# Performance work log

Hardware: AMD Instinct MI355X
Metric: run time of the kernel (lower is better)

## Reference

```python
import jax, jax.numpy as jnp
import numpy as np

N_NODES = 100000
N_EDGES = 1600000
IN_DIM = 128
HID = 32
HEADS = 4
NUM_CLASS = 2


def setup_inputs() -> dict:
    key = jax.random.key(0)
    ks = jax.random.split(key, 10)
    x = jax.random.normal(ks[0], (N_NODES, IN_DIM), dtype=jnp.float32)
    edge_index = jax.random.randint(ks[1], (2, N_EDGES), 0, N_NODES, dtype=jnp.int64)
    s_in = 1.0 / np.sqrt(IN_DIM)
    s_h = 1.0 / np.sqrt(HEADS * HID)
    return {
        "x": x,
        "edge_index": edge_index,
        "W1": jax.random.normal(ks[2], (HEADS * HID, IN_DIM), dtype=jnp.float32) * s_in,
        "att_src1": jax.random.normal(ks[3], (HEADS, HID), dtype=jnp.float32) * s_in,
        "att_dst1": jax.random.normal(ks[4], (HEADS, HID), dtype=jnp.float32) * s_in,
        "b1": jnp.zeros((HEADS * HID,), dtype=jnp.float32),
        "W2": jax.random.normal(ks[5], (NUM_CLASS, HEADS * HID), dtype=jnp.float32) * s_h,
        "att_src2": jax.random.normal(ks[6], (1, NUM_CLASS), dtype=jnp.float32) * s_h,
        "att_dst2": jax.random.normal(ks[7], (1, NUM_CLASS), dtype=jnp.float32) * s_h,
        "b2": jnp.zeros((NUM_CLASS,), dtype=jnp.float32),
    }


def gat_conv(x, src, dst, W, att_src, att_dst, b, n):
    """PyG-style GATConv (self-loops already included in src/dst)."""
    H, C = att_src.shape
    h = (x @ W.T).reshape(n, H, C)                      # [N,H,C]
    a_s = jnp.einsum('nhc,hc->nh', h, att_src)           # [N,H]
    a_d = jnp.einsum('nhc,hc->nh', h, att_dst)           # [N,H]
    e = jax.nn.leaky_relu(a_s[src] + a_d[dst], 0.2)      # [E,H]
    m = jax.ops.segment_max(e, dst, num_segments=n)      # per-dst max
    m = jnp.where(jnp.isfinite(m), m, 0.0)
    ex = jnp.exp(e - m[dst])
    denom = jax.ops.segment_sum(ex, dst, num_segments=n)
    alpha = ex / (denom[dst] + 1e-16)                    # segment softmax
    out = jax.ops.segment_sum(h[src] * alpha[..., None], dst, num_segments=n)
    return out.reshape(n, H * C) + b


def reference(x, edge_index, W1, att_src1, att_dst1, b1, W2, att_src2, att_dst2, b2):
    n = x.shape[0]
    loops = jnp.arange(n, dtype=edge_index.dtype)
    ei = jnp.concatenate([edge_index, jnp.stack([loops, loops])], axis=1)
    src, dst = ei[0], ei[1]
    h = gat_conv(x, src, dst, W1, att_src1, att_dst1, b1, n)
    h = jax.nn.leaky_relu(h, 0.01)  # F.leaky_relu default slope
    # F.dropout with p=0.0 -> identity
    out = gat_conv(h, src, dst, W2, att_src2, att_dst2, b2, n)
    return jax.nn.log_softmax(out, axis=1)
```

## Files before the change

### kernel.cpp

```cpp
#include <hip/hip_runtime.h>

#define NN 100000
#define NE 1600000
#define NTOT (NN + NE)
#define NB 782
#define ACHUNK 4096
#define NCH 391
#define BCAP 3072

typedef __attribute__((ext_vector_type(8))) short bf16x8;
typedef __attribute__((ext_vector_type(4))) float f32x4;

static __device__ __forceinline__ float blo(unsigned int u) {
  union { unsigned int i; float f; } v; v.i = u << 16; return v.f;
}
static __device__ __forceinline__ float bhi(unsigned int u) {
  union { unsigned int i; float f; } v; v.i = u & 0xffff0000u; return v.f;
}
static __device__ __forceinline__ unsigned short f2bf(float f) {
  union { float f; unsigned int i; } v; v.f = f;
  unsigned int i = v.i;
  i += 0x7fffu + ((i >> 16) & 1u);
  return (unsigned short)(i >> 16);
}

__global__ __launch_bounds__(512) void kb_hist(const int* __restrict__ ei,
                                               int* __restrict__ cntMat) {
  __shared__ int h[NB];
  int tid = threadIdx.x, blk = blockIdx.x;
  int e0 = blk * ACHUNK;
  int n = min(ACHUNK, NE - e0);
  for (int i = tid; i < NB; i += 512) h[i] = 0;
  __syncthreads();
  for (int i = tid; i < n; i += 512) atomicAdd(&h[ei[NE + e0 + i] >> 7], 1);
  __syncthreads();
  for (int i = tid; i < NB; i += 512) cntMat[blk * NB + i] = h[i];
}

__global__ void kb_colscan(int* __restrict__ cntMat, int* __restrict__ bucketCnt) {
  int b = blockIdx.x;
  int lane = threadIdx.x;
  int carry = 0;
  for (int base = 0; base < NCH; base += 64) {
    int idx = base + lane;
    int v = (idx < NCH) ? cntMat[idx * NB + b] : 0;
    int x = v;
#pragma unroll
    for (int d = 1; d < 64; d <<= 1) {
      int y = __shfl_up(x, d, 64);
      if (lane >= d) x += y;
    }
    if (idx < NCH) cntMat[idx * NB + b] = carry + x - v;
    carry += __shfl(x, 63, 64);
  }
  if (lane == 0) bucketCnt[b] = carry;
}

__global__ void kb_scan(const int* __restrict__ bucketCnt, int* __restrict__ pairOffset) {
  int lane = threadIdx.x;
  int c[13];
  int run = 0;
  int idx0 = lane * 13;
#pragma unroll
  for (int k = 0; k < 13; ++k) {
    int idx = idx0 + k;
    int v = (idx < NB) ? bucketCnt[idx] : 0;
    c[k] = run;
    run += v;
  }
  int x = run;
#pragma unroll
  for (int d = 1; d < 64; d <<= 1) {
    int y = __shfl_up(x, d, 64);
    if (lane >= d) x += y;
  }
  int laneoff = x - run;
#pragma unroll
  for (int k = 0; k < 13; ++k) {
    int idx = idx0 + k;
    if (idx <= NB) pairOffset[idx] = laneoff + c[k];
  }
}

__global__ __launch_bounds__(512) void kb_scatA(const int* __restrict__ ei,
                                                const int* __restrict__ pairOffset,
                                                const int* __restrict__ cntMat,
                                                int* __restrict__ pair) {
  __shared__ int lcnt[NB + 1];
  __shared__ int gbase[NB];
  __shared__ int lcur[NB];
  __shared__ int stage[ACHUNK];
  int tid = threadIdx.x, blk = blockIdx.x;
  int e0 = blk * ACHUNK;
  int n = min(ACHUNK, NE - e0);
  for (int i = tid; i <= NB; i += 512) lcnt[i] = 0;
  __syncthreads();
  for (int i = tid; i < n; i += 512) atomicAdd(&lcnt[ei[NE + e0 + i] >> 7], 1);
  __syncthreads();
  if (tid < 64) {
    int c[13];
    int run = 0;
    int idx0 = tid * 13;
#pragma unroll
    for (int k = 0; k < 13; ++k) {
      int idx = idx0 + k;
      int v = (idx < NB) ? lcnt[idx] : 0;
      c[k] = run;
      run += v;
    }
    int x = run;
#pragma unroll
    for (int d = 1; d < 64; d <<= 1) {
      int y = __shfl_up(x, d, 64);
      if (tid >= d) x += y;
    }
    int laneoff = x - run;
#pragma unroll
    for (int k = 0; k < 13; ++k) {
      int idx = idx0 + k;
      if (idx <= NB) lcnt[idx] = laneoff + c[k];
    }
  }
  __syncthreads();
  for (int b = tid; b < NB; b += 512) {
    gbase[b] = pairOffset[b] + cntMat[blk * NB + b];
    lcur[b] = lcnt[b];
  }
  __syncthreads();
  for (int i = tid; i < n; i += 512) {
    int s = ei[e0 + i], d = ei[NE + e0 + i];
    int b = d >> 7;
    int p = atomicAdd(&lcur[b], 1);
    stage[p] = (s << 7) | (d & 127);
  }
  __syncthreads();
  for (int b = tid; b < NB; b += 512) {
    int base = lcnt[b], cnt = lcnt[b + 1] - base, g = gbase[b];
    for (int k = 0; k < cnt; ++k) pair[g + k] = stage[base + k];
  }
}

__global__ __launch_bounds__(256) void kb_binB(const int* __restrict__ pair,
                                               const int* __restrict__ pairOffset,
                                               int* __restrict__ rowptr,
                                               int* __restrict__ col) {
  __shared__ int cnt[128];
  __shared__ int cur[128];
  __shared__ int stage[BCAP];
  int tid = threadIdx.x;
  int b = blockIdx.x;
  int dbase = b << 7;
  int nd = min(128, NN - dbase);
  int pbeg = pairOffset[b], m = pairOffset[b + 1] - pbeg;
  int cbase = pbeg + dbase;
  if (tid < 128) cnt[tid] = 0;
  __syncthreads();
  for (int i = tid; i < m; i += 256) atomicAdd(&cnt[pair[pbeg + i] & 127], 1);
  __syncthreads();
  if (tid < 64) {
    int i0 = 2 * tid, i1 = 2 * tid + 1;
    int v0 = cnt[i0] + (i0 < nd ? 1 : 0);
    int v1 = cnt[i1] + (i1 < nd ? 1 : 0);
    int run = v0 + v1;
    int x = run;
#pragma unroll
    for (int d = 1; d < 64; d <<= 1) {
      int y = __shfl_up(x, d, 64);
      if (tid >= d) x += y;
    }
    int e0 = x - run;
    int e1 = e0 + v0;
    if (i0 < nd) { rowptr[dbase + i0] = cbase + e0; stage[e0] = dbase + i0; cur[i0] = e0 + 1; }
    else cur[i0] = e0;
    if (i1 < nd) { rowptr[dbase + i1] = cbase + e1; stage[e1] = dbase + i1; cur[i1] = e1 + 1; }
    else cur[i1] = e1;
  }
  if (b == NB - 1 && tid == 0) rowptr[NN] = NTOT;
  __syncthreads();
  for (int i = tid; i < m; i += 256) {
    int p = pair[pbeg + i];
    int pos = atomicAdd(&cur[p & 127], 1);
    stage[pos] = p >> 7;
  }
  __syncthreads();
  int tot = m + nd;
  for (int i = tid; i < tot; i += 256) col[cbase + i] = stage[i];
}

__global__ void k_cvtW(const float* __restrict__ W1, unsigned short* __restrict__ Whp,
                       unsigned short* __restrict__ Wlp) {
  int i = blockIdx.x * 256 + threadIdx.x;
  if (i < 128 * 128) {
    int row = i >> 7, k = i & 127;
    int ot = row >> 4, r16 = row & 15;
    int c = k >> 5, quad = (k >> 3) & 3, j = k & 7;
    int dst = ((ot * 4 + c) * 64 + quad * 16 + r16) * 8 + j;
    float v = W1[i];
    unsigned short h = f2bf(v);
    Whp[dst] = h;
    Wlp[dst] = f2bf(v - blo((unsigned int)h));
  }
}

__global__ __launch_bounds__(256, 5) void k_gemm1(
    const float* __restrict__ x, const unsigned short* __restrict__ Whp,
    const unsigned short* __restrict__ Wlp, const float* __restrict__ asrc,
    const float* __restrict__ adst, unsigned short* __restrict__ h1b,
    float4* __restrict__ as1, float4* __restrict__ ad1) {
  __shared__ float xs[4][16 * 129];
  int wid = threadIdx.x >> 6, lane = threadIdx.x & 63;
  int tile = blockIdx.x * 4 + wid;
  if (tile >= NN / 16) tile = NN / 16 - 1;
  int r16 = lane & 15, quad = lane >> 4;
  const float4* xg = (const float4*)(x + (size_t)tile * 16 * 128);
  {
    int half = lane >> 5, l32 = lane & 31;
#pragma unroll
    for (int i = 0; i < 8; ++i) {
      int row = i * 2 + half;
      float4 v = xg[row * 32 + l32];
      float* dp = &xs[wid][row * 129 + l32 * 4];
      dp[0] = v.x; dp[1] = v.y; dp[2] = v.z; dp[3] = v.w;
    }
  }
  bf16x8 ah[4], al[4];
  const float* xr = &xs[wid][r16 * 129 + quad * 8];
#pragma unroll
  for (int c = 0; c < 4; ++c) {
#pragma unroll
    for (int j = 0; j < 8; ++j) {
      float v = xr[c * 32 + j];
      union { float f; unsigned int i; } u; u.f = v;
      ah[c][j] = (short)(u.i >> 16);
      union { float f; unsigned int i; } l; l.f = v - bhi(u.i);
      al[c][j] = (short)(l.i >> 16);
    }
  }
  float asp[4][4], adp[4][4];
#pragma unroll
  for (int h = 0; h < 4; ++h)
#pragma unroll
    for (int r = 0; r < 4; ++r) { asp[h][r] = 0.f; adp[h][r] = 0.f; }
#pragma unroll
  for (int ot = 0; ot < 8; ++ot) {
    f32x4 acc = {0.f, 0.f, 0.f, 0.f};
#pragma unroll
    for (int c = 0; c < 4; ++c) {
      const bf16x8 wh = *(const bf16x8*)(Whp + ((size_t)(ot * 4 + c) * 64 + lane) * 8);
      const bf16x8 wl = *(const bf16x8*)(Wlp + ((size_t)(ot * 4 + c) * 64 + lane) * 8);
      acc = __builtin_amdgcn_mfma_f32_16x16x32_bf16(ah[c], wh, acc, 0, 0, 0);
      acc = __builtin_amdgcn_mfma_f32_16x16x32_bf16(ah[c], wl, acc, 0, 0, 0);
      acc = __builtin_amdgcn_mfma_f32_16x16x32_bf16(al[c], wh, acc, 0, 0, 0);
    }
    float sa = asrc[ot * 16 + r16], da = adst[ot * 16 + r16];
    const int hh = ot >> 1;
#pragma unroll
    for (int r = 0; r < 4; ++r) {
      asp[hh][r] += acc[r] * sa;
      adp[hh][r] += acc[r] * da;
    }
    unsigned short* o = h1b + (size_t)(tile * 16 + quad * 4) * 128 + ot * 16 + r16;
    o[0] = f2bf(acc[0]); o[128] = f2bf(acc[1]);
    o[256] = f2bf(acc[2]); o[384] = f2bf(acc[3]);
  }
#pragma unroll
  for (int h = 0; h < 4; ++h)
#pragma unroll
    for (int r = 0; r < 4; ++r) {
      float v = asp[h][r];
      v += __shfl_xor(v, 1, 64); v += __shfl_xor(v, 2, 64);
      v += __shfl_xor(v, 4, 64); v += __shfl_xor(v, 8, 64);
      asp[h][r] = v;
      float w = adp[h][r];
      w += __shfl_xor(w, 1, 64); w += __shfl_xor(w, 2, 64);
      w += __shfl_xor(w, 4, 64); w += __shfl_xor(w, 8, 64);
      adp[h][r] = w;
    }
#pragma unroll
  for (int r = 0; r < 4; ++r) {
    if (r16 == r) {
      int node = tile * 16 + quad * 4 + r;
      as1[node] = make_float4(asp[0][r], asp[1][r], asp[2][r], asp[3][r]);
      ad1[node] = make_float4(adp[0][r], adp[1][r], adp[2][r], adp[3][r]);
    }
  }
}

__global__ __launch_bounds__(256, 6) void k_agg1(
    const unsigned short* __restrict__ h1b, const float* __restrict__ as1,
    const float* __restrict__ ad1, const int* __restrict__ rowptr,
    const int* __restrict__ col, const float* __restrict__ b1,
    const float* __restrict__ W2, const float* __restrict__ asrc2,
    const float* __restrict__ adst2, float4* __restrict__ node2) {
  int wid = threadIdx.x >> 6, lane = threadIdx.x & 63;
  int grp = lane >> 4, l16 = lane & 15;
  int node = blockIdx.x * 16 + wid * 4 + grp;
  int head = l16 >> 2;
  float ad = ad1[node * 4 + head];
  int beg = rowptr[node], deg = rowptr[node + 1] - beg;
  const uint4* h1q = (const uint4*)h1b;
  float acc[8] = {0.f, 0.f, 0.f, 0.f, 0.f, 0.f, 0.f, 0.f};
  float wsum = 0.f;
  int j = 0;
  while (__ballot(j < deg)) {
    bool a[8]; int s[8];
#pragma unroll
    for (int k = 0; k < 8; ++k) {
      a[k] = (j + k) < deg;
      s[k] = a[k] ? col[beg + j + k] : 0;
    }
    float e[8]; uint4 u[8];
#pragma unroll
    for (int k = 0; k < 8; ++k) e[k] = as1[s[k] * 4 + head] + ad;
#pragma unroll
    for (int k = 0; k < 8; ++k) u[k] = h1q[(size_t)s[k] * 16 + l16];
#pragma unroll
    for (int k = 0; k < 8; ++k) {
      float t = e[k];
      t = (t < 0.f) ? 0.2f * t : t;
      float w = a[k] ? __expf(fminf(t, 80.f)) : 0.f;
      wsum += w;
      acc[0] += w * blo(u[k].x); acc[1] += w * bhi(u[k].x);
      acc[2] += w * blo(u[k].y); acc[3] += w * bhi(u[k].y);
      acc[4] += w * blo(u[k].z); acc[5] += w * bhi(u[k].z);
      acc[6] += w * blo(u[k].w); acc[7] += w * bhi(u[k].w);
    }
    j += 8;
  }
  float inv = 1.f / (wsum + 1e-16f);
  int cb = l16 * 8;
  float h[8];
#pragma unroll
  for (int t = 0; t < 8; ++t) {
    float v = acc[t] * inv + b1[cb + t];
    h[t] = (v < 0.f) ? 0.01f * v : v;
  }
  float p0 = 0.f, p1 = 0.f;
#pragma unroll
  for (int t = 0; t < 8; ++t) {
    p0 += h[t] * W2[cb + t];
    p1 += h[t] * W2[128 + cb + t];
  }
  p0 += __shfl_xor(p0, 1, 64); p0 += __shfl_xor(p0, 2, 64);
  p0 += __shfl_xor(p0, 4, 64); p0 += __shfl_xor(p0, 8, 64);
  p1 += __shfl_xor(p1, 1, 64); p1 += __shfl_xor(p1, 2, 64);
  p1 += __shfl_xor(p1, 4, 64); p1 += __shfl_xor(p1, 8, 64);
  if (l16 == 0) {
    float as2 = p0 * asrc2[0] + p1 * asrc2[1];
    float ad2 = p0 * adst2[0] + p1 * adst2[1];
    node2[node] = make_float4(p0, p1, as2, ad2);
  }
}

__global__ void k_agg2(const float4* __restrict__ node2, const int* __restrict__ rowptr,
                       const int* __restrict__ col, const float* __restrict__ b2,
                       float2* __restrict__ out) {
  int t = blockIdx.x * 256 + threadIdx.x;
  int node = t >> 2, sub = t & 3;
  if (node >= NN) return;
  float ad2 = node2[node].w;
  int beg = rowptr[node], end = rowptr[node + 1];
  float den = 0.f, a0 = 0.f, a1 = 0.f;
  for (int j = beg + sub; j < end; j += 4) {
    int s = col[j];
    float4 sv = node2[s];
    float e = sv.z + ad2;
    e = (e < 0.f) ? 0.2f * e : e;
    float w = __expf(fminf(e, 80.f));
    den += w;
    a0 += w * sv.x;
    a1 += w * sv.y;
  }
#pragma unroll
  for (int d = 1; d < 4; d <<= 1) {
    den += __shfl_xor(den, d, 64);
    a0 += __shfl_xor(a0, d, 64);
    a1 += __shfl_xor(a1, d, 64);
  }
  if (sub == 0) {
    float inv = 1.f / (den + 1e-16f);
    float o0 = a0 * inv + b2[0];
    float o1 = a1 * inv + b2[1];
    float m = fmaxf(o0, o1);
    float lse = m + __logf(__expf(o0 - m) + __expf(o1 - m));
    out[node] = make_float2(o0 - lse, o1 - lse);
  }
}

extern "C" void kernel_launch(void* const* d_in, const int* in_sizes, int n_in,
                              void* d_out, int out_size, void* d_ws, size_t ws_size,
                              hipStream_t stream) {
  const float* x     = (const float*)d_in[0];
  const int*   ei    = (const int*)d_in[1];
  const float* W1    = (const float*)d_in[2];
  const float* asrc1 = (const float*)d_in[3];
  const float* adst1 = (const float*)d_in[4];
  const float* b1    = (const float*)d_in[5];
  const float* W2    = (const float*)d_in[6];
  const float* asrc2 = (const float*)d_in[7];
  const float* adst2 = (const float*)d_in[8];
  const float* b2    = (const float*)d_in[9];
  float2* out = (float2*)d_out;

  int* rowptr     = (int*)d_ws;
  int* col        = rowptr + 100352;
  int* pair       = col + 1700096;
  int* cntMat     = pair + 1600000;
  int* bucketCnt  = cntMat + 305792;
  int* pairOffset = bucketCnt + 1024;
  unsigned short* h1b = (unsigned short*)(pairOffset + 1024);
  float*  as1  = (float*)(h1b + (size_t)NN * 128);
  float*  ad1  = as1 + NN * 4;
  float4* node2 = (float4*)(ad1 + NN * 4);
  unsigned short* W1h = (unsigned short*)(node2 + NN);
  unsigned short* W1l = W1h + 16384;

  kb_hist<<<NCH, 512, 0, stream>>>(ei, cntMat);
  kb_colscan<<<NB, 64, 0, stream>>>(cntMat, bucketCnt);
  kb_scan<<<1, 64, 0, stream>>>(bucketCnt, pairOffset);
  kb_scatA<<<NCH, 512, 0, stream>>>(ei, pairOffset, cntMat, pair);
  kb_binB<<<NB, 256, 0, stream>>>(pair, pairOffset, rowptr, col);
  k_cvtW<<<64, 256, 0, stream>>>(W1, W1h, W1l);
  k_gemm1<<<(NN / 16 + 3) / 4, 256, 0, stream>>>(x, W1h, W1l, asrc1, adst1, h1b,
                                                 (float4*)as1, (float4*)ad1);
  k_agg1<<<NN / 16, 256, 0, stream>>>(h1b, as1, ad1, rowptr, col, b1, W2, asrc2, adst2, node2);
  k_agg2<<<(NN * 4 + 255) / 256, 256, 0, stream>>>(node2, rowptr, col, b2, out);
}
```

Baseline: 251.4 us.

## Transpose GEMM MFMA operands, halve histogram chunk size, widen agg2 lanes

The first GEMM swaps MFMA operands so each lane holds four consecutive output channels of one node. That allows packed 8-byte bf16 stores of h1 and a shorter cross-lane reduction for the attention logits. The edge-sort histogram now uses 2048-edge chunks, doubling the chunk count and the count-matrix workspace, which gives more parallelism in the binning passes. The second aggregation assigns 8 lanes per node instead of 4 to spread each node's neighbor loop more widely, at the cost of more shuffles and idle lanes on low-degree nodes.

```diff
diff --git a/kernel.cpp b/kernel.cpp
--- a/kernel.cpp
+++ b/kernel.cpp
@@ -4,8 +4,8 @@
 #define NE 1600000
 #define NTOT (NN + NE)
 #define NB 782
-#define ACHUNK 4096
-#define NCH 391
+#define ACHUNK 2048
+#define NCH 782
 #define BCAP 3072
 
 typedef __attribute__((ext_vector_type(8))) short bf16x8;
@@ -223,7 +223,7 @@
       dp[0] = v.x; dp[1] = v.y; dp[2] = v.z; dp[3] = v.w;
     }
   }
-  bf16x8 ah[4], al[4];
+  bf16x8 bh[4], bl[4];
   const float* xr = &xs[wid][r16 * 129 + quad * 8];
 #pragma unroll
   for (int c = 0; c < 4; ++c) {
@@ -231,16 +231,14 @@
     for (int j = 0; j < 8; ++j) {
       float v = xr[c * 32 + j];
       union { float f; unsigned int i; } u; u.f = v;
-      ah[c][j] = (short)(u.i >> 16);
+      bh[c][j] = (short)(u.i >> 16);
       union { float f; unsigned int i; } l; l.f = v - bhi(u.i);
-      al[c][j] = (short)(l.i >> 16);
-    }
-  }
-  float asp[4][4], adp[4][4];
-#pragma unroll
-  for (int h = 0; h < 4; ++h)
-#pragma unroll
-    for (int r = 0; r < 4; ++r) { asp[h][r] = 0.f; adp[h][r] = 0.f; }
+      bl[c][j] = (short)(l.i >> 16);
+    }
+  }
+  float asp[4] = {0.f, 0.f, 0.f, 0.f};
+  float adp[4] = {0.f, 0.f, 0.f, 0.f};
+  int node = tile * 16 + r16;
 #pragma unroll
   for (int ot = 0; ot < 8; ++ot) {
     f32x4 acc = {0.f, 0.f, 0.f, 0.f};
@@ -248,41 +246,30 @@
     for (int c = 0; c < 4; ++c) {
       const bf16x8 wh = *(const bf16x8*)(Whp + ((size_t)(ot * 4 + c) * 64 + lane) * 8);
       const bf16x8 wl = *(const bf16x8*)(Wlp + ((size_t)(ot * 4 + c) * 64 + lane) * 8);
-      acc = __builtin_amdgcn_mfma_f32_16x16x32_bf16(ah[c], wh, acc, 0, 0, 0);
-      acc = __builtin_amdgcn_mfma_f32_16x16x32_bf16(ah[c], wl, acc, 0, 0, 0);
-      acc = __builtin_amdgcn_mfma_f32_16x16x32_bf16(al[c], wh, acc, 0, 0, 0);
-    }
-    float sa = asrc[ot * 16 + r16], da = adst[ot * 16 + r16];
+      acc = __builtin_amdgcn_mfma_f32_16x16x32_bf16(wh, bh[c], acc, 0, 0, 0);
+      acc = __builtin_amdgcn_mfma_f32_16x16x32_bf16(wl, bh[c], acc, 0, 0, 0);
+      acc = __builtin_amdgcn_mfma_f32_16x16x32_bf16(wh, bl[c], acc, 0, 0, 0);
+    }
+    float4 sa = *(const float4*)(asrc + ot * 16 + quad * 4);
+    float4 da = *(const float4*)(adst + ot * 16 + quad * 4);
     const int hh = ot >> 1;
-#pragma unroll
-    for (int r = 0; r < 4; ++r) {
-      asp[hh][r] += acc[r] * sa;
-      adp[hh][r] += acc[r] * da;
-    }
-    unsigned short* o = h1b + (size_t)(tile * 16 + quad * 4) * 128 + ot * 16 + r16;
-    o[0] = f2bf(acc[0]); o[128] = f2bf(acc[1]);
-    o[256] = f2bf(acc[2]); o[384] = f2bf(acc[3]);
-  }
-#pragma unroll
-  for (int h = 0; h < 4; ++h)
-#pragma unroll
-    for (int r = 0; r < 4; ++r) {
-      float v = asp[h][r];
-      v += __shfl_xor(v, 1, 64); v += __shfl_xor(v, 2, 64);
-      v += __shfl_xor(v, 4, 64); v += __shfl_xor(v, 8, 64);
-      asp[h][r] = v;
-      float w = adp[h][r];
-      w += __shfl_xor(w, 1, 64); w += __shfl_xor(w, 2, 64);
-      w += __shfl_xor(w, 4, 64); w += __shfl_xor(w, 8, 64);
-      adp[h][r] = w;
-    }
-#pragma unroll
-  for (int r = 0; r < 4; ++r) {
-    if (r16 == r) {
-      int node = tile * 16 + quad * 4 + r;
-      as1[node] = make_float4(asp[0][r], asp[1][r], asp[2][r], asp[3][r]);
-      ad1[node] = make_float4(adp[0][r], adp[1][r], adp[2][r], adp[3][r]);
-    }
+    asp[hh] += acc[0] * sa.x + acc[1] * sa.y + acc[2] * sa.z + acc[3] * sa.w;
+    adp[hh] += acc[0] * da.x + acc[1] * da.y + acc[2] * da.z + acc[3] * da.w;
+    unsigned short* o = h1b + (size_t)node * 128 + ot * 16 + quad * 4;
+    unsigned int p01 = (unsigned int)f2bf(acc[0]) | ((unsigned int)f2bf(acc[1]) << 16);
+    unsigned int p23 = (unsigned int)f2bf(acc[2]) | ((unsigned int)f2bf(acc[3]) << 16);
+    *(uint2*)o = make_uint2(p01, p23);
+  }
+#pragma unroll
+  for (int h = 0; h < 4; ++h) {
+    asp[h] += __shfl_xor(asp[h], 16, 64);
+    asp[h] += __shfl_xor(asp[h], 32, 64);
+    adp[h] += __shfl_xor(adp[h], 16, 64);
+    adp[h] += __shfl_xor(adp[h], 32, 64);
+  }
+  if (lane < 16) {
+    as1[node] = make_float4(asp[0], asp[1], asp[2], asp[3]);
+    ad1[node] = make_float4(adp[0], adp[1], adp[2], adp[3]);
   }
 }
 
@@ -356,12 +343,12 @@
                        const int* __restrict__ col, const float* __restrict__ b2,
                        float2* __restrict__ out) {
   int t = blockIdx.x * 256 + threadIdx.x;
-  int node = t >> 2, sub = t & 3;
+  int node = t >> 3, sub = t & 7;
   if (node >= NN) return;
   float ad2 = node2[node].w;
   int beg = rowptr[node], end = rowptr[node + 1];
   float den = 0.f, a0 = 0.f, a1 = 0.f;
-  for (int j = beg + sub; j < end; j += 4) {
+  for (int j = beg + sub; j < end; j += 8) {
     int s = col[j];
     float4 sv = node2[s];
     float e = sv.z + ad2;
@@ -372,7 +359,7 @@
     a1 += w * sv.y;
   }
 #pragma unroll
-  for (int d = 1; d < 4; d <<= 1) {
+  for (int d = 1; d < 8; d <<= 1) {
     den += __shfl_xor(den, d, 64);
     a0 += __shfl_xor(a0, d, 64);
     a1 += __shfl_xor(a1, d, 64);
@@ -406,7 +393,7 @@
   int* col        = rowptr + 100352;
   int* pair       = col + 1700096;
   int* cntMat     = pair + 1600000;
-  int* bucketCnt  = cntMat + 305792;
+  int* bucketCnt  = cntMat + 611584;
   int* pairOffset = bucketCnt + 1024;
   unsigned short* h1b = (unsigned short*)(pairOffset + 1024);
   float*  as1  = (float*)(h1b + (size_t)NN * 128);
@@ -424,5 +411,5 @@
   k_gemm1<<<(NN / 16 + 3) / 4, 256, 0, stream>>>(x, W1h, W1l, asrc1, adst1, h1b,
                                                  (float4*)as1, (float4*)ad1);
   k_agg1<<<NN / 16, 256, 0, stream>>>(h1b, as1, ad1, rowptr, col, b1, W2, asrc2, adst2, node2);
-  k_agg2<<<(NN * 4 + 255) / 256, 256, 0, stream>>>(node2, rowptr, col, b2, out);
-}
+  k_agg2<<<(NN * 8 + 255) / 256, 256, 0, stream>>>(node2, rowptr, col, b2, out);
+}
```

Result: slower. 257.6 us (+2.5%).
